# Kernel optimization log

Hardware: AMD Instinct MI355X
Metric: run time of the kernel (lower is better)

Reference implementation:

```python
import jax, jax.numpy as jnp
import numpy as np
from jax import lax

V = 23       # vocab size (prime -> all nonzero scales invertible mod V)
H = 256      # hidden width of the strictly-causal masked layer
B, L = 512, 1024
TEMP = 1.0

_a = np.arange(V)
# one_hot_minus: out[k] = sum_a x[a] * shift[(a - k) % V]
MINUS_IDX = jnp.asarray((_a[None, :] - _a[:, None]) % V)  # [k, a] -> index into shift
# one_hot_multiply: T[s, k, a] = 1 if (s * a) % V == k
MUL_T = jnp.asarray(np.equal.outer(np.outer(_a, _a) % V, _a).transpose(0, 2, 1).astype(np.float32))  # [s, k, a]
# multiplicative inverse mod V (Fermat: s^(V-2) mod V for prime V); inv(0) := 0
_inv = np.array([pow(int(s), V - 2, V) if s else 0 for s in range(V)])
INV_P = jnp.asarray((_inv[:, None] == _a[None, :]).astype(np.float32))  # [s, k]


def one_hot_argmax(x, temp):
    """Straight-through one-hot argmax (soft = softmax(x/temp))."""
    soft = jax.nn.softmax(x / temp, axis=-1)
    hard = jax.nn.one_hot(jnp.argmax(x, axis=-1), V, dtype=x.dtype)
    return soft + lax.stop_gradient(hard - soft)


def one_hot_minus(x, shift):
    # (x - shift) % V in one-hot space: out[k] = sum_a x[a] * shift[(a-k)%V]
    return jnp.einsum('ba,bka->bk', x, shift[:, MINUS_IDX])


def one_hot_multiply(x, scale):
    # (x * scale) % V in one-hot space
    return jnp.einsum('bs,ba,ska->bk', scale, x, MUL_T)


def setup_inputs() -> dict:
    key = jax.random.key(0)
    k1, k2, k3 = jax.random.split(key, 3)
    x_tokens = jax.random.randint(k1, (B, L), 0, V, dtype=jnp.int32)
    W1 = jax.random.normal(k2, (V, H), jnp.float32) * 0.1
    b1 = jnp.zeros((H,), jnp.float32)
    W2 = jax.random.normal(k3, (H, 2 * V), jnp.float32) * 0.1
    b2 = jnp.zeros((2 * V,), jnp.float32)
    return {"x_tokens": x_tokens, "W1": W1, "b1": b1, "W2": W2, "b2": b2}


def reference(x_tokens, W1, b1, W2, b2):
    x = jax.nn.one_hot(x_tokens, V, dtype=jnp.float32)  # [B, L, V] one-hot inputs

    def step(acc, x_t):
        # acc [B, V] = sum of previously generated one-hot outputs y[0..t-1];
        # this is exactly what the strictly-causal layer sees at position t,
        # so net_t equals layer(padded_inputs)[:, t, :] of the original loop.
        net = jax.nn.relu(acc @ W1 + b1) @ W2 + b2      # [B, 2V]
        loc = one_hot_argmax(net[:, :V], TEMP)
        scale = one_hot_argmax(net[:, V:], TEMP)
        inv_scale = scale @ INV_P                        # one-hot modular inverse
        out_t = one_hot_multiply(one_hot_minus(x_t, loc), inv_scale)
        return acc + out_t, out_t

    acc0 = jnp.zeros((x.shape[0], V), x.dtype)
    _, ys = lax.scan(step, acc0, jnp.swapaxes(x, 0, 1))  # scan over length
    return jnp.swapaxes(ys, 0, 1)                        # [B, L, V]
```

## Files before the change

### kernel.cpp

```cpp
#include <hip/hip_runtime.h>
#include <math.h>

#define V 23
#define HH 256
#define BB 512
#define LL 1024
#define NOUT 46

typedef float f32x2 __attribute__((ext_vector_type(2)));
typedef float f32x4 __attribute__((ext_vector_type(4)));

constexpr unsigned long long packInv(int lo) {
    const int inv[23] = {0,1,12,8,6,14,4,10,3,18,7,21,2,16,5,20,13,19,9,17,15,11,22};
    unsigned long long t = 0;
    for (int i = 0; i < 12; ++i) {
        int idx = lo + i;
        if (idx < 23) t |= (unsigned long long)inv[idx] << (5 * i);
    }
    return t;
}
constexpr unsigned long long INV_T0 = packInv(0);
constexpr unsigned long long INV_T1 = packInv(12);

#define DPPMAX(v, ctrl, rmask)                                                  \
    do {                                                                        \
        unsigned _t = (unsigned)__builtin_amdgcn_update_dpp(                    \
            (int)(v), (int)(v), (ctrl), (rmask), 0xF, false);                   \
        (v) = ((v) > _t) ? (v) : _t;                                            \
    } while (0)

__global__ __launch_bounds__(256, 2)
void daf_kernel(const int* __restrict__ xtok,
                const float* __restrict__ W1,
                const float* __restrict__ b1,
                const float* __restrict__ W2,
                const float* __restrict__ b2,
                float* __restrict__ out)
{
    __shared__ float sW1[V * HH];
    __shared__ float sV[HH];
    __shared__ float sP[2][4][64];
    __shared__ int   sTok[LL];
    __shared__ int   sK[LL];

    const int tid = threadIdx.x;
    const int w   = tid >> 6;
    const int l   = tid & 63;
    const int b   = blockIdx.x;

    for (int i = tid; i < V * HH; i += 256) sW1[i] = W1[i];
    for (int i = tid; i < LL; i += 256) sTok[i] = xtok[(size_t)b * LL + i];

    const bool activeA = (l < V);
    const bool activeB = (l >= 32 && l < 32 + V);
    const bool active  = activeA || activeB;
    const int  col     = activeA ? l : (activeB ? (l - 32 + V) : 0);

    double h_pre = (double)b1[tid];

    const float bias = active ? b2[col] : 0.f;

    f32x2 wreg2[32];
    #pragma unroll
    for (int ii = 0; ii < 32; ++ii) {
        wreg2[ii].x = active ? W2[(size_t)(64 * w + 2 * ii + 0) * NOUT + col] : 0.f;
        wreg2[ii].y = active ? W2[(size_t)(64 * w + 2 * ii + 1) * NOUT + col] : 0.f;
    }
    #pragma unroll
    for (int ii = 0; ii < 32; ++ii) asm volatile("" : "+v"(wreg2[ii]));

    __syncthreads();

    for (int t = 0; t < LL; ++t) {
        const int tok = sTok[t];

        float v = fmaxf((float)h_pre, 0.f);
        sV[tid] = v;

        const f32x4* pv = (const f32x4*)(sV + 64 * w);
        f32x2 A01 = {0.f, 0.f};
        f32x2 A23 = {0.f, 0.f};
        #pragma unroll
        for (int q = 0; q < 16; ++q) {
            f32x4 vv = pv[q];
            f32x2 vlo; vlo.x = vv.x; vlo.y = vv.y;
            f32x2 vhi; vhi.x = vv.z; vhi.y = vv.w;
            asm("v_pk_fma_f32 %0, %1, %2, %0" : "+v"(A01) : "v"(vlo), "v"(wreg2[2 * q + 0]));
            asm("v_pk_fma_f32 %0, %1, %2, %0" : "+v"(A23) : "v"(vhi), "v"(wreg2[2 * q + 1]));
        }
        const int p = t & 1;
        sP[p][w][l] = (A01.x + A01.y) + (A23.x + A23.y);
        __syncthreads();

        const float* pp = &sP[p][0][l];
        const float p0 = pp[0], p1 = pp[64], p2 = pp[128], p3 = pp[192];
        float net = bias + ((p0 + p1) + (p2 + p3));
        int ib = __float_as_int(net);
        unsigned monoraw = (ib < 0) ? ~(unsigned)ib : ((unsigned)ib ^ 0x80000000u);
        const unsigned orig = active ? monoraw : 0u;

        unsigned red = orig;
        DPPMAX(red, 0xB1,  0xF);
        DPPMAX(red, 0x4E,  0xF);
        DPPMAX(red, 0x141, 0xF);
        DPPMAX(red, 0x140, 0xF);
        DPPMAX(red, 0x142, 0xA);
        const unsigned sA = (unsigned)__builtin_amdgcn_readlane((int)red, 16);
        const unsigned sB = (unsigned)__builtin_amdgcn_readlane((int)red, 48);

        const unsigned cmpv = (l < 32) ? sA : sB;
        const unsigned long long bal = __ballot(orig == cmpv);
        const int loc = __builtin_ctzll(bal & 0xFFFFFFFFull);
        const int sc  = __builtin_ctzll(bal >> 32);

        const unsigned long long tt = (sc < 12) ? INV_T0 : INV_T1;
        const int sh  = 5 * (sc - ((sc >= 12) ? 12 : 0));
        const int inv = (int)((tt >> sh) & 31);

        int m = tok - loc;
        m += (m >> 31) & V;
        const int k = (m * inv) % V;

        h_pre += (double)sW1[k * HH + tid];
        if (tid == 0) sK[t] = k;
    }

    __syncthreads();
    float* outb = out + (size_t)b * LL * V;
    for (int t = tid; t < LL; t += 256)
        outb[t * V + sK[t]] = 1.0f;
}

extern "C" void kernel_launch(void* const* d_in, const int* in_sizes, int n_in,
                              void* d_out, int out_size, void* d_ws, size_t ws_size,
                              hipStream_t stream) {
    const int*   xtok = (const int*)d_in[0];
    const float* W1   = (const float*)d_in[1];
    const float* b1   = (const float*)d_in[2];
    const float* W2   = (const float*)d_in[3];
    const float* b2   = (const float*)d_in[4];
    float* out = (float*)d_out;

    hipMemsetAsync(out, 0, (size_t)out_size * sizeof(float), stream);
    daf_kernel<<<BB, 256, 0, stream>>>(xtok, W1, b1, W2, b2, out);
}
```

Measured before the change: 687.4 us.

## Shrink block to two waves, each covering 128 hidden units

```diff
diff --git a/kernel.cpp b/kernel.cpp
--- a/kernel.cpp
+++ b/kernel.cpp
@@ -29,7 +29,7 @@
         (v) = ((v) > _t) ? (v) : _t;                                            \
     } while (0)
 
-__global__ __launch_bounds__(256, 2)
+__global__ __launch_bounds__(128, 1)
 void daf_kernel(const int* __restrict__ xtok,
                 const float* __restrict__ W1,
                 const float* __restrict__ b1,
@@ -39,62 +39,74 @@
 {
     __shared__ float sW1[V * HH];
     __shared__ float sV[HH];
-    __shared__ float sP[2][4][64];
+    __shared__ float sP[2][2][64];
     __shared__ int   sTok[LL];
     __shared__ int   sK[LL];
 
     const int tid = threadIdx.x;
-    const int w   = tid >> 6;
+    const int wv  = tid >> 6;
     const int l   = tid & 63;
     const int b   = blockIdx.x;
 
-    for (int i = tid; i < V * HH; i += 256) sW1[i] = W1[i];
-    for (int i = tid; i < LL; i += 256) sTok[i] = xtok[(size_t)b * LL + i];
+    for (int i = tid; i < V * HH; i += 128) sW1[i] = W1[i];
+    for (int i = tid; i < LL; i += 128) sTok[i] = xtok[(size_t)b * LL + i];
 
     const bool activeA = (l < V);
     const bool activeB = (l >= 32 && l < 32 + V);
     const bool active  = activeA || activeB;
     const int  col     = activeA ? l : (activeB ? (l - 32 + V) : 0);
 
-    double h_pre = (double)b1[tid];
+    const int hbase = 128 * wv + 2 * l;
+    double h0 = (double)b1[hbase + 0];
+    double h1 = (double)b1[hbase + 1];
 
     const float bias = active ? b2[col] : 0.f;
 
-    f32x2 wreg2[32];
+    f32x2 wreg2[64];
     #pragma unroll
-    for (int ii = 0; ii < 32; ++ii) {
-        wreg2[ii].x = active ? W2[(size_t)(64 * w + 2 * ii + 0) * NOUT + col] : 0.f;
-        wreg2[ii].y = active ? W2[(size_t)(64 * w + 2 * ii + 1) * NOUT + col] : 0.f;
+    for (int ii = 0; ii < 64; ++ii) {
+        const int r = 128 * wv + 2 * ii;
+        wreg2[ii].x = active ? W2[(size_t)(r + 0) * NOUT + col] : 0.f;
+        wreg2[ii].y = active ? W2[(size_t)(r + 1) * NOUT + col] : 0.f;
     }
     #pragma unroll
-    for (int ii = 0; ii < 32; ++ii) asm volatile("" : "+v"(wreg2[ii]));
+    for (int ii = 0; ii < 64; ++ii) asm volatile("" : "+v"(wreg2[ii]));
 
     __syncthreads();
 
     for (int t = 0; t < LL; ++t) {
         const int tok = sTok[t];
 
-        float v = fmaxf((float)h_pre, 0.f);
-        sV[tid] = v;
+        f32x2 hv;
+        hv.x = fmaxf((float)h0, 0.f);
+        hv.y = fmaxf((float)h1, 0.f);
+        *(f32x2*)(sV + hbase) = hv;
 
-        const f32x4* pv = (const f32x4*)(sV + 64 * w);
-        f32x2 A01 = {0.f, 0.f};
-        f32x2 A23 = {0.f, 0.f};
+        const f32x4* pv = (const f32x4*)(sV + 128 * wv);
+        f32x2 A01a = {0.f, 0.f}, A23a = {0.f, 0.f};
+        f32x2 A01b = {0.f, 0.f}, A23b = {0.f, 0.f};
         #pragma unroll
         for (int q = 0; q < 16; ++q) {
-            f32x4 vv = pv[q];
-            f32x2 vlo; vlo.x = vv.x; vlo.y = vv.y;
-            f32x2 vhi; vhi.x = vv.z; vhi.y = vv.w;
-            asm("v_pk_fma_f32 %0, %1, %2, %0" : "+v"(A01) : "v"(vlo), "v"(wreg2[2 * q + 0]));
-            asm("v_pk_fma_f32 %0, %1, %2, %0" : "+v"(A23) : "v"(vhi), "v"(wreg2[2 * q + 1]));
+            f32x4 va = pv[q];
+            f32x4 vb = pv[16 + q];
+            f32x2 valo = __builtin_shufflevector(va, va, 0, 1);
+            f32x2 vahi = __builtin_shufflevector(va, va, 2, 3);
+            f32x2 vblo = __builtin_shufflevector(vb, vb, 0, 1);
+            f32x2 vbhi = __builtin_shufflevector(vb, vb, 2, 3);
+            asm("v_pk_fma_f32 %0, %1, %2, %0" : "+v"(A01a) : "v"(valo), "v"(wreg2[2 * q + 0]));
+            asm("v_pk_fma_f32 %0, %1, %2, %0" : "+v"(A23a) : "v"(vahi), "v"(wreg2[2 * q + 1]));
+            asm("v_pk_fma_f32 %0, %1, %2, %0" : "+v"(A01b) : "v"(vblo), "v"(wreg2[32 + 2 * q + 0]));
+            asm("v_pk_fma_f32 %0, %1, %2, %0" : "+v"(A23b) : "v"(vbhi), "v"(wreg2[32 + 2 * q + 1]));
         }
+        const float s_a = (A01a.x + A01a.y) + (A23a.x + A23a.y);
+        const float s_b = (A01b.x + A01b.y) + (A23b.x + A23b.y);
         const int p = t & 1;
-        sP[p][w][l] = (A01.x + A01.y) + (A23.x + A23.y);
+        sP[p][wv][l] = s_a + s_b;
         __syncthreads();
 
         const float* pp = &sP[p][0][l];
-        const float p0 = pp[0], p1 = pp[64], p2 = pp[128], p3 = pp[192];
-        float net = bias + ((p0 + p1) + (p2 + p3));
+        const float u0 = pp[0], u1 = pp[64];
+        float net = bias + (u0 + u1);
         int ib = __float_as_int(net);
         unsigned monoraw = (ib < 0) ? ~(unsigned)ib : ((unsigned)ib ^ 0x80000000u);
         const unsigned orig = active ? monoraw : 0u;
@@ -121,13 +133,15 @@
         m += (m >> 31) & V;
         const int k = (m * inv) % V;
 
-        h_pre += (double)sW1[k * HH + tid];
+        const f32x2 w1v = *(const f32x2*)(sW1 + k * HH + hbase);
+        h0 += (double)w1v.x;
+        h1 += (double)w1v.y;
         if (tid == 0) sK[t] = k;
     }
 
     __syncthreads();
     float* outb = out + (size_t)b * LL * V;
-    for (int t = tid; t < LL; t += 256)
+    for (int t = tid; t < LL; t += 128)
         outb[t * V + sK[t]] = 1.0f;
 }
 
@@ -142,5 +156,5 @@
     float* out = (float*)d_out;
 
     hipMemsetAsync(out, 0, (size_t)out_size * sizeof(float), stream);
-    daf_kernel<<<BB, 256, 0, stream>>>(xtok, W1, b1, W2, b2, out);
+    daf_kernel<<<BB, 128, 0, stream>>>(xtok, W1, b1, W2, b2, out);
 }
```

New measurement: 939.7 us. +36.7%, slower.

## Process two batch rows per block to interleave independent recurrences

Applied to the files above, without the earlier changes.

```diff
diff --git a/kernel.cpp b/kernel.cpp
--- a/kernel.cpp
+++ b/kernel.cpp
@@ -29,7 +29,31 @@
         (v) = ((v) > _t) ? (v) : _t;                                            \
     } while (0)
 
-__global__ __launch_bounds__(256, 2)
+__device__ __forceinline__ int pick_k(float net, bool active, int l, int tok) {
+    int ib = __float_as_int(net);
+    unsigned monoraw = (ib < 0) ? ~(unsigned)ib : ((unsigned)ib ^ 0x80000000u);
+    const unsigned orig = active ? monoraw : 0u;
+    unsigned red = orig;
+    DPPMAX(red, 0xB1,  0xF);
+    DPPMAX(red, 0x4E,  0xF);
+    DPPMAX(red, 0x141, 0xF);
+    DPPMAX(red, 0x140, 0xF);
+    DPPMAX(red, 0x142, 0xA);
+    const unsigned sA = (unsigned)__builtin_amdgcn_readlane((int)red, 16);
+    const unsigned sB = (unsigned)__builtin_amdgcn_readlane((int)red, 48);
+    const unsigned cmpv = (l < 32) ? sA : sB;
+    const unsigned long long bal = __ballot(orig == cmpv);
+    const int loc = __builtin_ctzll(bal & 0xFFFFFFFFull);
+    const int sc  = __builtin_ctzll(bal >> 32);
+    const unsigned long long tt = (sc < 12) ? INV_T0 : INV_T1;
+    const int sh  = 5 * (sc - ((sc >= 12) ? 12 : 0));
+    const int inv = (int)((tt >> sh) & 31);
+    int m = tok - loc;
+    m += (m >> 31) & V;
+    return (m * inv) % V;
+}
+
+__global__ __launch_bounds__(256, 1)
 void daf_kernel(const int* __restrict__ xtok,
                 const float* __restrict__ W1,
                 const float* __restrict__ b1,
@@ -38,10 +62,10 @@
                 float* __restrict__ out)
 {
     __shared__ float sW1[V * HH];
-    __shared__ float sV[HH];
-    __shared__ float sP[2][4][64];
-    __shared__ int   sTok[LL];
-    __shared__ int   sK[LL];
+    __shared__ float sV[2][HH];
+    __shared__ float sP[2][2][4][64];
+    __shared__ int   sTok[2][LL];
+    __shared__ int   sK[2][LL];
 
     const int tid = threadIdx.x;
     const int w   = tid >> 6;
@@ -49,14 +73,18 @@
     const int b   = blockIdx.x;
 
     for (int i = tid; i < V * HH; i += 256) sW1[i] = W1[i];
-    for (int i = tid; i < LL; i += 256) sTok[i] = xtok[(size_t)b * LL + i];
+    for (int i = tid; i < LL; i += 256) {
+        sTok[0][i] = xtok[(size_t)(2 * b + 0) * LL + i];
+        sTok[1][i] = xtok[(size_t)(2 * b + 1) * LL + i];
+    }
 
     const bool activeA = (l < V);
     const bool activeB = (l >= 32 && l < 32 + V);
     const bool active  = activeA || activeB;
     const int  col     = activeA ? l : (activeB ? (l - 32 + V) : 0);
 
-    double h_pre = (double)b1[tid];
+    double hA = (double)b1[tid];
+    double hB = (double)b1[tid];
 
     const float bias = active ? b2[col] : 0.f;
 
@@ -72,63 +100,55 @@
     __syncthreads();
 
     for (int t = 0; t < LL; ++t) {
-        const int tok = sTok[t];
+        const int tokA = sTok[0][t];
+        const int tokB = sTok[1][t];
 
-        float v = fmaxf((float)h_pre, 0.f);
-        sV[tid] = v;
+        sV[0][tid] = fmaxf((float)hA, 0.f);
+        sV[1][tid] = fmaxf((float)hB, 0.f);
 
-        const f32x4* pv = (const f32x4*)(sV + 64 * w);
-        f32x2 A01 = {0.f, 0.f};
-        f32x2 A23 = {0.f, 0.f};
+        const f32x4* pvA = (const f32x4*)(sV[0] + 64 * w);
+        const f32x4* pvB = (const f32x4*)(sV[1] + 64 * w);
+        f32x2 A01 = {0.f, 0.f}, A23 = {0.f, 0.f};
+        f32x2 B01 = {0.f, 0.f}, B23 = {0.f, 0.f};
         #pragma unroll
         for (int q = 0; q < 16; ++q) {
-            f32x4 vv = pv[q];
-            f32x2 vlo; vlo.x = vv.x; vlo.y = vv.y;
-            f32x2 vhi; vhi.x = vv.z; vhi.y = vv.w;
-            asm("v_pk_fma_f32 %0, %1, %2, %0" : "+v"(A01) : "v"(vlo), "v"(wreg2[2 * q + 0]));
-            asm("v_pk_fma_f32 %0, %1, %2, %0" : "+v"(A23) : "v"(vhi), "v"(wreg2[2 * q + 1]));
+            f32x4 va = pvA[q];
+            f32x4 vb = pvB[q];
+            f32x2 valo = __builtin_shufflevector(va, va, 0, 1);
+            f32x2 vahi = __builtin_shufflevector(va, va, 2, 3);
+            f32x2 vblo = __builtin_shufflevector(vb, vb, 0, 1);
+            f32x2 vbhi = __builtin_shufflevector(vb, vb, 2, 3);
+            asm("v_pk_fma_f32 %0, %1, %2, %0" : "+v"(A01) : "v"(valo), "v"(wreg2[2 * q + 0]));
+            asm("v_pk_fma_f32 %0, %1, %2, %0" : "+v"(A23) : "v"(vahi), "v"(wreg2[2 * q + 1]));
+            asm("v_pk_fma_f32 %0, %1, %2, %0" : "+v"(B01) : "v"(vblo), "v"(wreg2[2 * q + 0]));
+            asm("v_pk_fma_f32 %0, %1, %2, %0" : "+v"(B23) : "v"(vbhi), "v"(wreg2[2 * q + 1]));
         }
         const int p = t & 1;
-        sP[p][w][l] = (A01.x + A01.y) + (A23.x + A23.y);
+        sP[p][0][w][l] = (A01.x + A01.y) + (A23.x + A23.y);
+        sP[p][1][w][l] = (B01.x + B01.y) + (B23.x + B23.y);
         __syncthreads();
 
-        const float* pp = &sP[p][0][l];
-        const float p0 = pp[0], p1 = pp[64], p2 = pp[128], p3 = pp[192];
-        float net = bias + ((p0 + p1) + (p2 + p3));
-        int ib = __float_as_int(net);
-        unsigned monoraw = (ib < 0) ? ~(unsigned)ib : ((unsigned)ib ^ 0x80000000u);
-        const unsigned orig = active ? monoraw : 0u;
+        const float* ppA = &sP[p][0][0][l];
+        const float* ppB = &sP[p][1][0][l];
+        const float qa0 = ppA[0], qa1 = ppA[64], qa2 = ppA[128], qa3 = ppA[192];
+        const float qb0 = ppB[0], qb1 = ppB[64], qb2 = ppB[128], qb3 = ppB[192];
+        const float netA = bias + ((qa0 + qa1) + (qa2 + qa3));
+        const float netB = bias + ((qb0 + qb1) + (qb2 + qb3));
 
-        unsigned red = orig;
-        DPPMAX(red, 0xB1,  0xF);
-        DPPMAX(red, 0x4E,  0xF);
-        DPPMAX(red, 0x141, 0xF);
-        DPPMAX(red, 0x140, 0xF);
-        DPPMAX(red, 0x142, 0xA);
-        const unsigned sA = (unsigned)__builtin_amdgcn_readlane((int)red, 16);
-        const unsigned sB = (unsigned)__builtin_amdgcn_readlane((int)red, 48);
+        const int kA = pick_k(netA, active, l, tokA);
+        const int kB = pick_k(netB, active, l, tokB);
 
-        const unsigned cmpv = (l < 32) ? sA : sB;
-        const unsigned long long bal = __ballot(orig == cmpv);
-        const int loc = __builtin_ctzll(bal & 0xFFFFFFFFull);
-        const int sc  = __builtin_ctzll(bal >> 32);
-
-        const unsigned long long tt = (sc < 12) ? INV_T0 : INV_T1;
-        const int sh  = 5 * (sc - ((sc >= 12) ? 12 : 0));
-        const int inv = (int)((tt >> sh) & 31);
-
-        int m = tok - loc;
-        m += (m >> 31) & V;
-        const int k = (m * inv) % V;
-
-        h_pre += (double)sW1[k * HH + tid];
-        if (tid == 0) sK[t] = k;
+        hA += (double)sW1[kA * HH + tid];
+        hB += (double)sW1[kB * HH + tid];
+        if (tid == 0) { sK[0][t] = kA; sK[1][t] = kB; }
     }
 
     __syncthreads();
-    float* outb = out + (size_t)b * LL * V;
-    for (int t = tid; t < LL; t += 256)
-        outb[t * V + sK[t]] = 1.0f;
+    for (int s = 0; s < 2; ++s) {
+        float* outb = out + (size_t)(2 * b + s) * LL * V;
+        for (int t = tid; t < LL; t += 256)
+            outb[t * V + sK[s][t]] = 1.0f;
+    }
 }
 
 extern "C" void kernel_launch(void* const* d_in, const int* in_sizes, int n_in,
@@ -142,5 +162,5 @@
     float* out = (float*)d_out;
 
     hipMemsetAsync(out, 0, (size_t)out_size * sizeof(float), stream);
-    daf_kernel<<<BB, 256, 0, stream>>>(xtok, W1, b1, W2, b2, out);
+    daf_kernel<<<BB / 2, 256, 0, stream>>>(xtok, W1, b1, W2, b2, out);
 }
```

Measured after the change: 1.064 ms. 1.55x slower.
